# Kernel optimization log

Hardware: AMD Instinct MI355X
Metric: run time of the kernel (lower is better)

The kernel has to match this reference:

```python
import jax, jax.numpy as jnp
import numpy as np

EPS = 1e-5

def layer_norm(x, w, b):
    mu = jnp.mean(x, axis=-1, keepdims=True)
    var = jnp.var(x, axis=-1, keepdims=True)
    return (x - mu) * jax.lax.rsqrt(var + EPS) * w + b

def setup_inputs() -> dict:
    key = jax.random.key(0)
    ks = jax.random.split(key, 9)
    B, N, d, hidden = 1, 512, 64, 128
    s = 0.02
    return {
        "z": jax.random.normal(ks[0], (B, N, N, d), dtype=jnp.float32),
        "ln_in_w": jnp.ones((d,), jnp.float32),
        "ln_in_b": jnp.zeros((d,), jnp.float32),
        "Wp": jax.random.normal(ks[1], (d, 2 * hidden), jnp.float32) * s,
        "Wg": jax.random.normal(ks[2], (d, 2 * hidden), jnp.float32) * s,
        "ln_out_w": jnp.ones((hidden,), jnp.float32),
        "ln_out_b": jnp.zeros((hidden,), jnp.float32),
        "Wout": jax.random.normal(ks[3], (hidden, d), jnp.float32) * s,
        "Wgate": jax.random.normal(ks[4], (d, d), jnp.float32) * s,
    }

def reference(z, ln_in_w, ln_in_b, Wp, Wg, ln_out_w, ln_out_b, Wout, Wgate):
    # z: [B, N, N, d]
    h = layer_norm(z, ln_in_w, ln_in_b)
    p = h @ Wp                               # [B,N,N,2*hidden]
    g_in = jax.nn.sigmoid(h @ Wg)            # [B,N,N,2*hidden]
    pg = p * g_in
    a, b = jnp.split(pg, 2, axis=-1)         # each [B,N,N,hidden]
    # direction == 'outgoing'
    out = jnp.einsum('bikd,bjkd->bijd', a, b)  # [B,N,N,hidden]
    out = layer_norm(out, ln_out_w, ln_out_b)
    g_out = jax.nn.sigmoid(h @ Wgate)        # [B,N,N,d]
    return (out @ Wout) * g_out              # [B,N,N,d]
```

## Files before the change

kernel.cpp:

```cpp
#include <hip/hip_runtime.h>
#include <hip/hip_fp16.h>


typedef _Float16 half_t;
typedef _Float16 f16x4 __attribute__((ext_vector_type(4)));
typedef _Float16 f16x8 __attribute__((ext_vector_type(8)));
typedef float f32x4 __attribute__((ext_vector_type(4)));

#define NSEQ 512
#define HID 128
#define ROWS (NSEQ * NSEQ)

#define GLOAD16(src, dst)                                                        \
    __builtin_amdgcn_global_load_lds(                                            \
        (const __attribute__((address_space(1))) void*)(src),                    \
        (__attribute__((address_space(3))) void*)(dst), 16, 0, 0)

__device__ __forceinline__ float fast_sigmoid(float x) {
    float e = __builtin_amdgcn_exp2f(-1.44269504088896f * x);
    return __builtin_amdgcn_rcpf(1.f + e);
}

__global__ void k_prep_w(const float* __restrict__ Wp, const float* __restrict__ Wg,
                         const float* __restrict__ Wgate,
                         const float* __restrict__ ln_out_w, const float* __restrict__ ln_out_b,
                         const float* __restrict__ Wout,
                         half_t* __restrict__ Wimg, half_t* __restrict__ W1t,
                         float* __restrict__ s1, float* __restrict__ s2) {
    int bid = blockIdx.x, t = threadIdx.x;
    if (bid < 18) {
        int chunk = bid * 256 + t;
        int ch = chunk >= 2304;
        int q = chunk - ch * 2304;
        int lr = q >> 3, slot = q & 7;
        int co = slot ^ (lr & 7);
        int grow;
        if (lr < 128)      grow = ch * 128 + lr;
        else if (lr < 256) grow = 256 + ch * 128 + (lr - 128);
        else               grow = 512 + ch * 32 + (lr - 256);
        f16x8 vals;
        #pragma unroll
        for (int j = 0; j < 8; ++j) {
            int l = co * 8 + j;
            float v;
            if (grow < 256)      v = Wp[l * 256 + grow];
            else if (grow < 512) v = Wg[l * 256 + (grow - 256)];
            else                 v = Wgate[l * 64 + (grow - 512)];
            vals[j] = (half_t)v;
        }
        *(f16x8*)(Wimg + (size_t)chunk * 8) = vals;
    } else {
        #pragma unroll
        for (int i = 0; i < 32; ++i) {
            int idx = t * 32 + i;
            int o = idx >> 7, c = idx & 127;
            W1t[idx] = (half_t)(ln_out_w[c] * Wout[c * 64 + o]);
        }
        if (t < 64) {
            float a1 = 0.f, a2 = 0.f;
            for (int c = 0; c < 128; ++c) {
                float wo = Wout[c * 64 + t];
                a1 += ln_out_w[c] * wo;
                a2 += ln_out_b[c] * wo;
            }
            s1[t] = a1; s2[t] = a2;
        }
    }
}

__global__ __launch_bounds__(256) void k_ln_in(const float* __restrict__ z,
                                               const float* __restrict__ w,
                                               const float* __restrict__ b,
                                               half_t* __restrict__ h) {
    int t = threadIdx.x;
    int row = blockIdx.x * 16 + (t >> 4);
    int c4 = t & 15;
    f32x4 x = *(const f32x4*)(z + (size_t)row * 64 + c4 * 4);
    float s = x[0] + x[1] + x[2] + x[3];
    float s2 = x[0]*x[0] + x[1]*x[1] + x[2]*x[2] + x[3]*x[3];
    #pragma unroll
    for (int off = 1; off < 16; off <<= 1) {
        s  += __shfl_xor(s,  off, 64);
        s2 += __shfl_xor(s2, off, 64);
    }
    float mu = s * (1.f / 64.f);
    float var = s2 * (1.f / 64.f) - mu * mu;
    float rs = rsqrtf(var + 1e-5f);
    f32x4 wv = *(const f32x4*)(w + c4 * 4);
    f32x4 bv = *(const f32x4*)(b + c4 * 4);
    f16x4 o;
    #pragma unroll
    for (int j = 0; j < 4; ++j)
        o[j] = (half_t)((x[j] - mu) * rs * wv[j] + bv[j]);
    *(f16x4*)(h + (size_t)row * 64 + c4 * 4) = o;
}

__global__ __launch_bounds__(256) void k_proj(const half_t* __restrict__ h,
                                              const half_t* __restrict__ Wimg,
                                              half_t* __restrict__ a_t,
                                              half_t* __restrict__ b_t,
                                              half_t* __restrict__ g_out) {
    __shared__ half_t Wl[288 * 64];
    __shared__ half_t pgl[64 * 66];

    int t = threadIdx.x;
    int ch = blockIdx.y;
    int bx = blockIdx.x;
    int r0 = bx * 64;
    int wid = t >> 6, lane = t & 63;
    int m = lane & 15, g = lane >> 4;

    const half_t* wsrc = Wimg + (size_t)ch * 2304 * 8;
    #pragma unroll
    for (int it = 0; it < 9; ++it) {
        int cb = it * 256 + wid * 64;
        GLOAD16(wsrc + (size_t)(cb + lane) * 8, Wl + (size_t)cb * 8);
    }

    int growbase = r0 + wid * 16;
    f16x8 af[2];
    #pragma unroll
    for (int ks = 0; ks < 2; ++ks)
        af[ks] = *(const f16x8*)(h + (size_t)(growbase + m) * 64 + ks * 32 + g * 8);

    __syncthreads();

    half_t* dst = (ch == 0) ? a_t : b_t;
    int sw = (bx >> 3) & 7;

    for (int grp = 0; grp < 2; ++grp) {
        #pragma unroll
        for (int pt4 = 0; pt4 < 4; ++pt4) {
            int pt = grp * 4 + pt4;
            f32x4 accp = {0.f, 0.f, 0.f, 0.f}, accg = {0.f, 0.f, 0.f, 0.f};
            #pragma unroll
            for (int ks = 0; ks < 2; ++ks) {
                int kb = (ks * 32 + g * 8) * 2;
                int lrp = pt * 16 + m;
                f16x8 bp = *(const f16x8*)((char*)Wl + lrp * 128 + (kb ^ ((lrp & 7) << 4)));
                int lrg = 128 + pt * 16 + m;
                f16x8 bg = *(const f16x8*)((char*)Wl + lrg * 128 + (kb ^ ((lrg & 7) << 4)));
                accp = __builtin_amdgcn_mfma_f32_16x16x32_f16(af[ks], bp, accp, 0, 0, 0);
                accg = __builtin_amdgcn_mfma_f32_16x16x32_f16(af[ks], bg, accg, 0, 0, 0);
            }
            f16x4 pk;
            #pragma unroll
            for (int r = 0; r < 4; ++r)
                pk[r] = (half_t)(accp[r] * fast_sigmoid(accg[r]));
            *(f16x4*)&pgl[(pt4 * 16 + m) * 66 + wid * 16 + g * 4] = pk;
        }
        __syncthreads();
        #pragma unroll
        for (int it = 0; it < 2; ++it) {
            int chunk = it * 256 + t;
            int cl = chunk >> 3, r8 = chunk & 7;
            f16x8 v = *(const f16x8*)&pgl[cl * 66 + r8 * 8];
            *(f16x8*)(dst + (size_t)(grp * 64 + cl) * ROWS + r0 + (r8 ^ sw) * 8) = v;
        }
        __syncthreads();
    }

    for (int gt = 0; gt < 2; ++gt) {
        f32x4 acc = {0.f, 0.f, 0.f, 0.f};
        #pragma unroll
        for (int ks = 0; ks < 2; ++ks) {
            int kb = (ks * 32 + g * 8) * 2;
            int lr = 256 + gt * 16 + m;
            f16x8 bb = *(const f16x8*)((char*)Wl + lr * 128 + (kb ^ ((lr & 7) << 4)));
            acc = __builtin_amdgcn_mfma_f32_16x16x32_f16(af[ks], bb, acc, 0, 0, 0);
        }
        int och = ch * 32 + gt * 16 + m;
        #pragma unroll
        for (int r = 0; r < 4; ++r) {
            float og = fast_sigmoid(acc[r]);
            int grow = growbase + g * 4 + r;
            g_out[(size_t)grow * 64 + och] = (half_t)og;
        }
    }
}

__global__ __launch_bounds__(512) void k_einsum(const half_t* __restrict__ a_t,
                                                const half_t* __restrict__ b_t,
                                                half_t* __restrict__ out_mid) {
    __shared__ half_t Al[256 * 64];
    __shared__ half_t Bl[256 * 64];

    int t = threadIdx.x;
    int bid = blockIdx.x;
    int xcd = bid & 7, kk = bid >> 3;
    int c = xcd + 8 * (kk >> 2);
    int tt = kk & 3;
    int i0 = (tt & 1) * 256, j0 = (tt >> 1) * 256;

    const half_t* A = a_t + (size_t)c * ROWS;
    const half_t* B = b_t + (size_t)c * ROWS;

    int wid = t >> 6, lane = t & 63;
    int m = lane & 15, g = lane >> 4;
    int wr = wid >> 2, wc = wid & 3;

    f32x4 acc[8][4] = {};

    for (int kt = 0; kt < 8; ++kt) {
        __syncthreads();
        #pragma unroll
        for (int rnd = 0; rnd < 4; ++rnd) {
            int cb = rnd * 512 + wid * 64;
            int chunk = cb + lane;
            int row = chunk >> 3, slot = chunk & 7;
            const half_t* ga = A + (size_t)(i0 + row) * 512 + kt * 64 + slot * 8;
            const half_t* gb = B + (size_t)(j0 + row) * 512 + kt * 64 + slot * 8;
            GLOAD16(ga, Al + (size_t)cb * 8);
            GLOAD16(gb, Bl + (size_t)cb * 8);
        }
        __syncthreads();

        #pragma unroll
        for (int ks = 0; ks < 2; ++ks) {
            int kb = (ks * 32 + g * 8) * 2;
            f16x8 bf[4];
            #pragma unroll
            for (int ni = 0; ni < 4; ++ni) {
                int lrow = wc * 64 + ni * 16 + m;
                bf[ni] = *(const f16x8*)((char*)Bl + lrow * 128 + (kb ^ ((lrow & 7) << 4)));
            }
            #pragma unroll
            for (int mi = 0; mi < 8; ++mi) {
                int lrow = wr * 128 + mi * 16 + m;
                f16x8 afr = *(const f16x8*)((char*)Al + lrow * 128 + (kb ^ ((lrow & 7) << 4)));
                #pragma unroll
                for (int ni = 0; ni < 4; ++ni)
                    acc[mi][ni] = __builtin_amdgcn_mfma_f32_16x16x32_f16(afr, bf[ni], acc[mi][ni], 0, 0, 0);
            }
        }
    }

    half_t* O = out_mid + (size_t)c * ROWS;
    #pragma unroll
    for (int mi = 0; mi < 8; ++mi) {
        #pragma unroll
        for (int ni = 0; ni < 4; ++ni) {
            int row = i0 + wr * 128 + mi * 16 + g * 4;
            int col = j0 + wc * 64 + ni * 16 + m;
            #pragma unroll
            for (int r = 0; r < 4; ++r)
                O[(size_t)(row + r) * 512 + col] = (half_t)acc[mi][ni][r];
        }
    }
}

__global__ __launch_bounds__(256) void k_final(const half_t* __restrict__ out_mid,
                                               const half_t* __restrict__ W1t,
                                               const float* __restrict__ s1g,
                                               const float* __restrict__ s2g,
                                               const half_t* __restrict__ g_out,
                                               float* __restrict__ out) {
    __shared__ half_t midl[128 * 64];
    __shared__ half_t midt[64 * 128];
    __shared__ half_t w1l[64 * 128];
    __shared__ half_t gl[64 * 72];
    __shared__ float smu[64], srs[64], s1l[64], s2l[64];

    int t = threadIdx.x;
    int pos0 = blockIdx.x * 64;

    #pragma unroll
    for (int it = 0; it < 4; ++it) {
        int chunk = it * 256 + t;
        int cc = chunk >> 3, co = chunk & 7;
        *(uint4*)((char*)midl + cc * 128 + co * 16) =
            *(const uint4*)(out_mid + (size_t)cc * ROWS + pos0 + co * 8);
    }
    #pragma unroll
    for (int it = 0; it < 4; ++it) {
        int chunk = it * 256 + t;
        int row = chunk >> 4, slot = chunk & 15;
        *(uint4*)((char*)w1l + row * 256 + ((slot * 16) ^ ((row & 7) << 4))) =
            *(const uint4*)(W1t + row * 128 + slot * 8);
    }
    #pragma unroll
    for (int it = 0; it < 2; ++it) {
        int chunk = it * 256 + t;
        int row = chunk >> 3, co = chunk & 7;
        *(uint4*)((char*)gl + row * 144 + co * 16) =
            *(const uint4*)(g_out + (size_t)(pos0 + row) * 64 + co * 8);
    }
    if (t < 64) { s1l[t] = s1g[t]; s2l[t] = s2g[t]; }
    __syncthreads();

    {
        int p = t >> 2, q = t & 3;
        float s = 0.f, s2 = 0.f;
        #pragma unroll
        for (int cc4 = 0; cc4 < 4; ++cc4) {
            f16x8 pack;
            #pragma unroll
            for (int j = 0; j < 8; ++j) {
                half_t hv = midl[(q * 32 + cc4 * 8 + j) * 64 + p];
                float v = (float)hv;
                s += v; s2 += v * v;
                pack[j] = hv;
            }
            int slot = q * 4 + cc4;
            *(f16x8*)((char*)midt + p * 256 + ((slot * 16) ^ ((p & 7) << 4))) = pack;
        }
        s  += __shfl_xor(s, 1, 64);  s  += __shfl_xor(s, 2, 64);
        s2 += __shfl_xor(s2, 1, 64); s2 += __shfl_xor(s2, 2, 64);
        if (q == 0) {
            float mu = s * (1.f / 128.f);
            float var = s2 * (1.f / 128.f) - mu * mu;
            smu[p] = mu;
            srs[p] = rsqrtf(var + 1e-5f);
        }
    }
    __syncthreads();

    int wid = t >> 6, lane = t & 63;
    int m = lane & 15, g = lane >> 4;

    f32x4 acc[4] = {};
    #pragma unroll
    for (int ks = 0; ks < 4; ++ks) {
        int arow = wid * 16 + m;
        f16x8 af = *(const f16x8*)((char*)midt + arow * 256 +
                                   (((4 * ks + g) * 16) ^ ((arow & 7) << 4)));
        #pragma unroll
        for (int ni = 0; ni < 4; ++ni) {
            int brow = ni * 16 + m;
            f16x8 bf = *(const f16x8*)((char*)w1l + brow * 256 +
                                       (((4 * ks + g) * 16) ^ ((brow & 7) << 4)));
            acc[ni] = __builtin_amdgcn_mfma_f32_16x16x32_f16(af, bf, acc[ni], 0, 0, 0);
        }
    }

    #pragma unroll
    for (int ni = 0; ni < 4; ++ni) {
        int o = ni * 16 + m;
        float v1 = s1l[o], v2 = s2l[o];
        #pragma unroll
        for (int r = 0; r < 4; ++r) {
            int lrow = wid * 16 + g * 4 + r;
            float mu = smu[lrow], rs = srs[lrow];
            float val = acc[ni][r] * rs - mu * rs * v1 + v2;
            float gate = (float)gl[lrow * 72 + o];
            out[(size_t)(pos0 + lrow) * 64 + o] = val * gate;
        }
    }
}

extern "C" void kernel_launch(void* const* d_in, const int* in_sizes, int n_in,
                              void* d_out, int out_size, void* d_ws, size_t ws_size,
                              hipStream_t stream) {
    const float* z        = (const float*)d_in[0];
    const float* ln_in_w  = (const float*)d_in[1];
    const float* ln_in_b  = (const float*)d_in[2];
    const float* Wp       = (const float*)d_in[3];
    const float* Wg       = (const float*)d_in[4];
    const float* ln_out_w = (const float*)d_in[5];
    const float* ln_out_b = (const float*)d_in[6];
    const float* Wout     = (const float*)d_in[7];
    const float* Wgate    = (const float*)d_in[8];
    float* out = (float*)d_out;

    char* wsb = (char*)d_ws;
    half_t* Wimg = (half_t*)wsb;
    half_t* W1t  = (half_t*)(wsb + 81920);
    float*  s1   = (float*)(wsb + 98304);
    float*  s2   = (float*)(wsb + 98560);
    half_t* a_t  = (half_t*)(wsb + 131072);
    half_t* b_t  = a_t + (size_t)HID * ROWS;
    half_t* gout = b_t + (size_t)HID * ROWS;
    half_t* omid = gout + (size_t)ROWS * 64;
    half_t* h    = omid;

    k_prep_w<<<dim3(19), dim3(256), 0, stream>>>(Wp, Wg, Wgate, ln_out_w, ln_out_b, Wout,
                                                 Wimg, W1t, s1, s2);
    k_ln_in<<<dim3(ROWS / 16), dim3(256), 0, stream>>>(z, ln_in_w, ln_in_b, h);
    k_proj<<<dim3(ROWS / 64, 2), dim3(256), 0, stream>>>(h, Wimg, a_t, b_t, gout);
    k_einsum<<<dim3(512), dim3(512), 0, stream>>>(a_t, b_t, omid);
    k_final<<<dim3(ROWS / 64), dim3(256), 0, stream>>>(omid, W1t, s1, s2, gout, out);
}
```

Baseline: 163.7 us.

## Double-buffer einsum K tiles with async LDS loads and adjust swizzle

The einsum kernel now splits K into 32-wide tiles held in two LDS buffers and prefetches the next tile with global_load_lds while MFMAs run on the current one, using explicit vmcnt waits and raw barriers. The producer kernel's swizzle of a_t/b_t columns changes to a 4-way XOR within 32-element halves so it matches the new 64-byte LDS row layout. This aims to hide global load latency behind compute. The cost is twice as many barriers per K step and hand-written waitcnt counts that must match the number of outstanding loads.

```diff
diff --git a/kernel.cpp b/kernel.cpp
--- a/kernel.cpp
+++ b/kernel.cpp
@@ -126,7 +126,7 @@
     __syncthreads();
 
     half_t* dst = (ch == 0) ? a_t : b_t;
-    int sw = (bx >> 3) & 7;
+    int swz = (bx >> 4) & 3;
 
     for (int grp = 0; grp < 2; ++grp) {
         #pragma unroll
@@ -155,7 +155,8 @@
             int chunk = it * 256 + t;
             int cl = chunk >> 3, r8 = chunk & 7;
             f16x8 v = *(const f16x8*)&pgl[cl * 66 + r8 * 8];
-            *(f16x8*)(dst + (size_t)(grp * 64 + cl) * ROWS + r0 + (r8 ^ sw) * 8) = v;
+            int dk = (r8 & 4) | ((r8 & 3) ^ swz);
+            *(f16x8*)(dst + (size_t)(grp * 64 + cl) * ROWS + r0 + dk * 8) = v;
         }
         __syncthreads();
     }
@@ -182,8 +183,8 @@
 __global__ __launch_bounds__(512) void k_einsum(const half_t* __restrict__ a_t,
                                                 const half_t* __restrict__ b_t,
                                                 half_t* __restrict__ out_mid) {
-    __shared__ half_t Al[256 * 64];
-    __shared__ half_t Bl[256 * 64];
+    __shared__ half_t Al[2][256 * 32];
+    __shared__ half_t Bl[2][256 * 32];
 
     int t = threadIdx.x;
     int bid = blockIdx.x;
@@ -201,39 +202,55 @@
 
     f32x4 acc[8][4] = {};
 
-    for (int kt = 0; kt < 8; ++kt) {
-        __syncthreads();
-        #pragma unroll
-        for (int rnd = 0; rnd < 4; ++rnd) {
-            int cb = rnd * 512 + wid * 64;
-            int chunk = cb + lane;
-            int row = chunk >> 3, slot = chunk & 7;
-            const half_t* ga = A + (size_t)(i0 + row) * 512 + kt * 64 + slot * 8;
-            const half_t* gb = B + (size_t)(j0 + row) * 512 + kt * 64 + slot * 8;
-            GLOAD16(ga, Al + (size_t)cb * 8);
-            GLOAD16(gb, Bl + (size_t)cb * 8);
-        }
-        __syncthreads();
-
-        #pragma unroll
-        for (int ks = 0; ks < 2; ++ks) {
-            int kb = (ks * 32 + g * 8) * 2;
-            f16x8 bf[4];
-            #pragma unroll
-            for (int ni = 0; ni < 4; ++ni) {
-                int lrow = wc * 64 + ni * 16 + m;
-                bf[ni] = *(const f16x8*)((char*)Bl + lrow * 128 + (kb ^ ((lrow & 7) << 4)));
-            }
-            #pragma unroll
-            for (int mi = 0; mi < 8; ++mi) {
-                int lrow = wr * 128 + mi * 16 + m;
-                f16x8 afr = *(const f16x8*)((char*)Al + lrow * 128 + (kb ^ ((lrow & 7) << 4)));
-                #pragma unroll
-                for (int ni = 0; ni < 4; ++ni)
-                    acc[mi][ni] = __builtin_amdgcn_mfma_f32_16x16x32_f16(afr, bf[ni], acc[mi][ni], 0, 0, 0);
-            }
-        }
-    }
+#define STAGE(ktt, Ab, Bb)                                                        \
+    {                                                                             \
+        _Pragma("unroll")                                                         \
+        for (int rnd = 0; rnd < 2; ++rnd) {                                       \
+            int cb = rnd * 512 + wid * 64;           \
+            int chunk = cb + lane;                                                \
+            int row = chunk >> 2, slot = chunk & 3;                               \
+            GLOAD16(A + (size_t)(i0 + row) * 512 + (ktt) * 32 + slot * 8,         \
+                    (Ab) + (size_t)cb * 8);                                       \
+            GLOAD16(B + (size_t)(j0 + row) * 512 + (ktt) * 32 + slot * 8,         \
+                    (Bb) + (size_t)cb * 8);                                       \
+        }                                                                         \
+    }
+
+    STAGE(0, Al[0], Bl[0]);
+
+    #pragma unroll 2
+    for (int kt = 0; kt < 16; ++kt) {
+        const int cur = kt & 1;
+        if (kt < 15) {
+            STAGE(kt + 1, Al[cur ^ 1], Bl[cur ^ 1]);
+            asm volatile("s_waitcnt vmcnt(4)" ::: "memory");
+        } else {
+            asm volatile("s_waitcnt vmcnt(0)" ::: "memory");
+        }
+        __builtin_amdgcn_s_barrier();
+        __builtin_amdgcn_sched_barrier(0);
+
+        const half_t* Ac = Al[cur];
+        const half_t* Bc = Bl[cur];
+        f16x8 bf[4];
+        #pragma unroll
+        for (int ni = 0; ni < 4; ++ni) {
+            int lrow = wc * 64 + ni * 16 + m;
+            int so = (g ^ ((lrow >> 1) & 3)) * 16;
+            bf[ni] = *(const f16x8*)((char*)Bc + lrow * 64 + so);
+        }
+        #pragma unroll
+        for (int mi = 0; mi < 8; ++mi) {
+            int lrow = wr * 128 + mi * 16 + m;
+            int so = (g ^ ((lrow >> 1) & 3)) * 16;
+            f16x8 afr = *(const f16x8*)((char*)Ac + lrow * 64 + so);
+            #pragma unroll
+            for (int ni = 0; ni < 4; ++ni)
+                acc[mi][ni] = __builtin_amdgcn_mfma_f32_16x16x32_f16(afr, bf[ni], acc[mi][ni], 0, 0, 0);
+        }
+        __builtin_amdgcn_s_barrier();
+    }
+#undef STAGE
 
     half_t* O = out_mid + (size_t)c * ROWS;
     #pragma unroll
```

After: 161.4 us. About the same (-1.4%).
